# Optimization experiments

Measured on AMD Instinct MI355X. Metric: run time of the kernel, lower is better.

Reference implementation:

```python
import jax, jax.numpy as jnp
import numpy as np

B, H, D, V = 1024, 4, 128, 100000
EPS = 1e-7  # keras backend epsilon used by SparseCategoricalCrossentropy clipping


def setup_inputs() -> dict:
    key = jax.random.key(0)
    k0, k1, k2, k3, k4 = jax.random.split(key, 5)
    inputs = jax.random.normal(k0, (B, D), dtype=jnp.float32)
    label = jax.random.randint(k1, (B,), 0, V)
    embeddings = jax.random.normal(k2, (V, D), dtype=jnp.float32) * 0.05
    proj_mat = jax.random.normal(k3, (H * D, D), dtype=jnp.float32) * 0.05
    mix_mat = jax.random.normal(k4, (H, D), dtype=jnp.float32) * 0.05
    return {"inputs": inputs, "label": label, "embeddings": embeddings,
            "proj_mat": proj_mat, "mix_mat": mix_mat}


def reference(inputs, label, embeddings, proj_mat, mix_mat):
    # proj: [B, H*D] -> [B, H, D] with tanh nonlinearity
    proj = jnp.tanh(inputs @ proj_mat.T).reshape(-1, H, D)
    # mixture weights pi: [B, H]
    pi = jax.nn.softmax(inputs @ mix_mat.T, axis=-1)
    # per-head full-vocab logits/probs: [B, H, V]
    head_logits = jnp.einsum('bhd,vd->bhv', proj, embeddings)
    head_probs = jax.nn.softmax(head_logits, axis=-1)
    # mixture of softmaxes: [B, V]
    probs = jnp.einsum('bh,bhv->bv', pi, head_probs)
    # sparse categorical cross-entropy on probabilities (not logits)
    p_label = jnp.take_along_axis(probs, label[:, None], axis=1)[:, 0]
    loss = -jnp.mean(jnp.log(jnp.clip(p_label, EPS, 1.0)))
    return probs, loss
```

## Files before the change

kernel.cpp:

```cpp
#include <hip/hip_runtime.h>
#include <hip/hip_bf16.h>
#include <math.h>

#define B_ 1024
#define H_ 4
#define D_ 128
#define V_ 100000
#define M_ (B_*H_)
#define EPS_ 1e-7f

typedef unsigned short ushort_t;
typedef __attribute__((ext_vector_type(4))) float f32x4;
typedef __attribute__((ext_vector_type(8))) short bf16x8;

__device__ __forceinline__ ushort_t f2bf(float f) {
    unsigned u = __float_as_uint(f);
    unsigned r = u + 0x7fffu + ((u >> 16) & 1u);
    return (ushort_t)(r >> 16);
}

__device__ __forceinline__ void gload_lds16(const void* g, void* l) {
    __builtin_amdgcn_global_load_lds(
        (const __attribute__((address_space(1))) unsigned int*)g,
        (__attribute__((address_space(3))) unsigned int*)l,
        16, 0, 0);
}

__global__ __launch_bounds__(512)
void proj_pi_kernel(const float* __restrict__ inputs, const float* __restrict__ proj_mat,
                    const float* __restrict__ mix_mat, ushort_t* __restrict__ Abf,
                    float* __restrict__ pi)
{
    __shared__ float xin[128];
    __shared__ float mixv[4];
    const int b = blockIdx.x, tid = threadIdx.x;
    if (tid < 128) xin[tid] = inputs[b * 128 + tid];
    __syncthreads();

    const float4* row = (const float4*)(proj_mat + tid * 128);
    float acc = 0.f;
#pragma unroll 8
    for (int k = 0; k < 32; ++k) {
        float4 m4 = row[k];
        acc += m4.x * xin[k*4+0] + m4.y * xin[k*4+1] + m4.z * xin[k*4+2] + m4.w * xin[k*4+3];
    }
    Abf[b * 512 + tid] = f2bf(tanhf(acc));

    if (tid < 4) {
        const float4* mrow = (const float4*)(mix_mat + tid * 128);
        float a2 = 0.f;
#pragma unroll 8
        for (int k = 0; k < 32; ++k) {
            float4 m4 = mrow[k];
            a2 += m4.x * xin[k*4+0] + m4.y * xin[k*4+1] + m4.z * xin[k*4+2] + m4.w * xin[k*4+3];
        }
        mixv[tid] = a2;
    }
    __syncthreads();
    if (tid < 4) {
        float m = fmaxf(fmaxf(mixv[0], mixv[1]), fmaxf(mixv[2], mixv[3]));
        float e0 = __expf(mixv[0]-m), e1 = __expf(mixv[1]-m), e2 = __expf(mixv[2]-m), e3 = __expf(mixv[3]-m);
        float s = e0 + e1 + e2 + e3;
        float mye = __expf(mixv[tid]-m);
        pi[b * 4 + tid] = mye / s;
    }
}

__global__ __launch_bounds__(256)
void conv_kernel(const float* __restrict__ e, ushort_t* __restrict__ o, int n4)
{
    int i = blockIdx.x * 256 + threadIdx.x;
    if (i < n4) {
        float4 f = ((const float4*)e)[i];
        ushort4 u;
        u.x = f2bf(f.x); u.y = f2bf(f.y); u.z = f2bf(f.z); u.w = f2bf(f.w);
        ((ushort4*)o)[i] = u;
    }
}

template <int PASS>
__global__ __launch_bounds__(256, 2)
void gemm_kernel(const ushort_t* __restrict__ Abf, const ushort_t* __restrict__ Ebf,
                 const float* __restrict__ pi, float* __restrict__ Z,
                 float* __restrict__ probs)
{
    __shared__ ushort_t lds_a[128 * 128];
    __shared__ ushort_t lds_b[128 * 128];
    __shared__ float w_lds[128];

    const int tid  = threadIdx.x;
    const int wave = tid >> 6;
    const int lane = tid & 63;
    const int q    = lane >> 4;
    const int r16  = lane & 15;
    const int m0   = blockIdx.x * 128;
    const int v0   = blockIdx.y * 128;

    if (PASS == 2) {
        if (tid < 128) {
            int gi = m0 + tid;
            w_lds[tid] = pi[gi] / Z[gi];
        }
    }

#pragma unroll
    for (int t = 0; t < 8; ++t) {
        int r  = t * 16 + (tid >> 4);
        int c  = tid & 15;
        int cs = c ^ (r & 7);
        unsigned loff = (unsigned)__builtin_amdgcn_readfirstlane(t * 4096 + (tid >> 6) * 1024);
        gload_lds16(Abf + (size_t)(m0 + r) * 128 + cs * 8, (char*)lds_a + loff);
        int vrow = v0 + r; if (vrow >= V_) vrow = V_ - 1;
        gload_lds16(Ebf + (size_t)vrow * 128 + cs * 8, (char*)lds_b + loff);
    }
    __syncthreads();

    const int wm = (wave >> 1) * 64;
    const int wn = (wave & 1) * 64;

    f32x4 acc[4][4];
#pragma unroll
    for (int mi = 0; mi < 4; ++mi)
#pragma unroll
        for (int ni = 0; ni < 4; ++ni)
            acc[mi][ni] = (f32x4)(0.f);

#pragma unroll
    for (int kk = 0; kk < 4; ++kk) {
        bf16x8 fa[4], fb[4];
        int chunk = kk * 4 + q;
#pragma unroll
        for (int mi = 0; mi < 4; ++mi) {
            int row = wm + mi * 16 + r16;
            int sc = chunk ^ (row & 7);
            fa[mi] = *(const bf16x8*)&lds_a[row * 128 + sc * 8];
        }
#pragma unroll
        for (int ni = 0; ni < 4; ++ni) {
            int row = wn + ni * 16 + r16;
            int sc = chunk ^ (row & 7);
            fb[ni] = *(const bf16x8*)&lds_b[row * 128 + sc * 8];
        }
#pragma unroll
        for (int mi = 0; mi < 4; ++mi)
#pragma unroll
            for (int ni = 0; ni < 4; ++ni)
                acc[mi][ni] = __builtin_amdgcn_mfma_f32_16x16x32_bf16(fa[mi], fb[ni], acc[mi][ni], 0, 0, 0);
    }

    if (PASS == 1) {
        float zs[4][4];
#pragma unroll
        for (int mi = 0; mi < 4; ++mi)
#pragma unroll
            for (int h = 0; h < 4; ++h) zs[mi][h] = 0.f;

#pragma unroll
        for (int mi = 0; mi < 4; ++mi) {
#pragma unroll
            for (int ni = 0; ni < 4; ++ni) {
                int v = v0 + wn + ni * 16 + r16;
                bool ok = (v < V_);
#pragma unroll
                for (int h = 0; h < 4; ++h) {
                    float e = ok ? __expf(acc[mi][ni][h]) : 0.f;
                    zs[mi][h] += e;
                }
            }
        }
#pragma unroll
        for (int msk = 1; msk < 16; msk <<= 1) {
#pragma unroll
            for (int mi = 0; mi < 4; ++mi)
#pragma unroll
                for (int h = 0; h < 4; ++h)
                    zs[mi][h] += __shfl_xor(zs[mi][h], msk, 64);
        }
        int mi = r16 >> 2, h = r16 & 3;
        int midx = m0 + wm + mi * 16 + q * 4 + h;
        atomicAdd(&Z[midx], zs[mi][h]);
    } else {
#pragma unroll
        for (int mi = 0; mi < 4; ++mi) {
            int mloc = wm + mi * 16 + q * 4;
            float w0 = w_lds[mloc + 0], w1 = w_lds[mloc + 1];
            float w2 = w_lds[mloc + 2], w3 = w_lds[mloc + 3];
            size_t rowoff = (size_t)((m0 + mloc) >> 2) * V_;
#pragma unroll
            for (int ni = 0; ni < 4; ++ni) {
                int v = v0 + wn + ni * 16 + r16;
                if (v < V_) {
                    f32x4 a = acc[mi][ni];
                    float p = w0 * __expf(a[0]) + w1 * __expf(a[1])
                            + w2 * __expf(a[2]) + w3 * __expf(a[3]);
                    probs[rowoff + v] = p;
                }
            }
        }
    }
}

__global__ __launch_bounds__(256)
void loss_kernel(const float* __restrict__ probs, const int* __restrict__ label,
                 float* __restrict__ out)
{
    __shared__ float red[256];
    int tid = threadIdx.x;
    float s = 0.f;
    for (int b = tid; b < B_; b += 256) {
        float p = probs[(size_t)b * V_ + label[b]];
        p = fminf(fmaxf(p, EPS_), 1.0f);
        s -= logf(p);
    }
    red[tid] = s;
    __syncthreads();
    for (int st = 128; st > 0; st >>= 1) {
        if (tid < st) red[tid] += red[tid + st];
        __syncthreads();
    }
    if (tid == 0) out[0] = red[0] / (float)B_;
}

extern "C" void kernel_launch(void* const* d_in, const int* in_sizes, int n_in,
                              void* d_out, int out_size, void* d_ws, size_t ws_size,
                              hipStream_t stream)
{
    const float* inputs   = (const float*)d_in[0];
    const int*   label    = (const int*)d_in[1];
    const float* emb      = (const float*)d_in[2];
    const float* proj_mat = (const float*)d_in[3];
    const float* mix_mat  = (const float*)d_in[4];
    float* out = (float*)d_out;

    char* ws = (char*)d_ws;
    ushort_t* emb_bf = (ushort_t*)ws;
    ushort_t* A_bf   = (ushort_t*)(ws + 25600000);
    float*    pi     = (float*)(ws + 26648576);
    float*    Z      = (float*)(ws + 26664960);

    conv_kernel<<<12500, 256, 0, stream>>>(emb, emb_bf, 3200000);
    proj_pi_kernel<<<1024, 512, 0, stream>>>(inputs, proj_mat, mix_mat, A_bf, pi);
    hipMemsetAsync(Z, 0, 4096 * sizeof(float), stream);

    dim3 g(32, 782);
    gemm_kernel<1><<<g, 256, 0, stream>>>(A_bf, emb_bf, nullptr, Z, nullptr);
    gemm_kernel<2><<<g, 256, 0, stream>>>(A_bf, emb_bf, pi, Z, out);

    loss_kernel<<<1, 256, 0, stream>>>(out, label, out + (size_t)B_ * V_);
}
```

Measured before the change: 829.5 us.

## Replace two-pass GEMM with single pass storing bf16 exp scores plus combine kernel

The logits GEMM now runs once, writing per-head exp scores as bf16 to a padded workspace buffer while accumulating the softmax normalisers. A separate combine kernel then applies pi/Z weights to produce probs. This removes the second GEMM and exp pass. In exchange it adds a large intermediate buffer that must be written and read back, and it rounds the exp values to bf16. log2e is folded into the bf16 embeddings so exp2 can be used.

Measured after the change: 1.036 ms. 24.9% more time.

```diff
diff --git a/kernel.cpp b/kernel.cpp
--- a/kernel.cpp
+++ b/kernel.cpp
@@ -6,8 +6,10 @@
 #define H_ 4
 #define D_ 128
 #define V_ 100000
+#define VP_ 100096
 #define M_ (B_*H_)
 #define EPS_ 1e-7f
+#define LOG2E_ 1.4426950408889634f
 
 typedef unsigned short ushort_t;
 typedef __attribute__((ext_vector_type(4))) float f32x4;
@@ -18,6 +20,8 @@
     unsigned r = u + 0x7fffu + ((u >> 16) & 1u);
     return (ushort_t)(r >> 16);
 }
+__device__ __forceinline__ float bf_lo(unsigned x) { return __uint_as_float(x << 16); }
+__device__ __forceinline__ float bf_hi(unsigned x) { return __uint_as_float(x & 0xffff0000u); }
 
 __device__ __forceinline__ void gload_lds16(const void* g, void* l) {
     __builtin_amdgcn_global_load_lds(
@@ -61,8 +65,7 @@
         float m = fmaxf(fmaxf(mixv[0], mixv[1]), fmaxf(mixv[2], mixv[3]));
         float e0 = __expf(mixv[0]-m), e1 = __expf(mixv[1]-m), e2 = __expf(mixv[2]-m), e3 = __expf(mixv[3]-m);
         float s = e0 + e1 + e2 + e3;
-        float mye = __expf(mixv[tid]-m);
-        pi[b * 4 + tid] = mye / s;
+        pi[b * 4 + tid] = __expf(mixv[tid]-m) / s;
     }
 }
 
@@ -73,20 +76,18 @@
     if (i < n4) {
         float4 f = ((const float4*)e)[i];
         ushort4 u;
-        u.x = f2bf(f.x); u.y = f2bf(f.y); u.z = f2bf(f.z); u.w = f2bf(f.w);
+        u.x = f2bf(f.x * LOG2E_); u.y = f2bf(f.y * LOG2E_);
+        u.z = f2bf(f.z * LOG2E_); u.w = f2bf(f.w * LOG2E_);
         ((ushort4*)o)[i] = u;
     }
 }
 
-template <int PASS>
 __global__ __launch_bounds__(256, 2)
-void gemm_kernel(const ushort_t* __restrict__ Abf, const ushort_t* __restrict__ Ebf,
-                 const float* __restrict__ pi, float* __restrict__ Z,
-                 float* __restrict__ probs)
+void gemm_s_kernel(const ushort_t* __restrict__ Abf, const ushort_t* __restrict__ Ebf,
+                   ushort_t* __restrict__ S, float* __restrict__ Z)
 {
     __shared__ ushort_t lds_a[128 * 128];
     __shared__ ushort_t lds_b[128 * 128];
-    __shared__ float w_lds[128];
 
     const int tid  = threadIdx.x;
     const int wave = tid >> 6;
@@ -95,13 +96,6 @@
     const int r16  = lane & 15;
     const int m0   = blockIdx.x * 128;
     const int v0   = blockIdx.y * 128;
-
-    if (PASS == 2) {
-        if (tid < 128) {
-            int gi = m0 + tid;
-            w_lds[tid] = pi[gi] / Z[gi];
-        }
-    }
 
 #pragma unroll
     for (int t = 0; t < 8; ++t) {
@@ -148,56 +142,60 @@
                 acc[mi][ni] = __builtin_amdgcn_mfma_f32_16x16x32_bf16(fa[mi], fb[ni], acc[mi][ni], 0, 0, 0);
     }
 
-    if (PASS == 1) {
-        float zs[4][4];
+    float zs[4][4];
+#pragma unroll
+    for (int mi = 0; mi < 4; ++mi)
+#pragma unroll
+        for (int h = 0; h < 4; ++h) zs[mi][h] = 0.f;
+
+#pragma unroll
+    for (int mi = 0; mi < 4; ++mi) {
+        int bidx = (m0 + wm + mi * 16) / 4 + q;
+#pragma unroll
+        for (int ni = 0; ni < 4; ++ni) {
+            int v = v0 + wn + ni * 16 + r16;
+            f32x4 a = acc[mi][ni];
+            float e0 = exp2f(a[0]), e1 = exp2f(a[1]), e2 = exp2f(a[2]), e3 = exp2f(a[3]);
+            ushort4 s4;
+            s4.x = f2bf(e0); s4.y = f2bf(e1); s4.z = f2bf(e2); s4.w = f2bf(e3);
+            *(ushort4*)(S + ((size_t)bidx * VP_ + v) * 4) = s4;
+            if (v < V_) {
+                zs[mi][0] += e0; zs[mi][1] += e1; zs[mi][2] += e2; zs[mi][3] += e3;
+            }
+        }
+    }
+#pragma unroll
+    for (int msk = 1; msk < 16; msk <<= 1) {
 #pragma unroll
         for (int mi = 0; mi < 4; ++mi)
 #pragma unroll
-            for (int h = 0; h < 4; ++h) zs[mi][h] = 0.f;
-
-#pragma unroll
-        for (int mi = 0; mi < 4; ++mi) {
-#pragma unroll
-            for (int ni = 0; ni < 4; ++ni) {
-                int v = v0 + wn + ni * 16 + r16;
-                bool ok = (v < V_);
-#pragma unroll
-                for (int h = 0; h < 4; ++h) {
-                    float e = ok ? __expf(acc[mi][ni][h]) : 0.f;
-                    zs[mi][h] += e;
-                }
-            }
-        }
-#pragma unroll
-        for (int msk = 1; msk < 16; msk <<= 1) {
-#pragma unroll
-            for (int mi = 0; mi < 4; ++mi)
-#pragma unroll
-                for (int h = 0; h < 4; ++h)
-                    zs[mi][h] += __shfl_xor(zs[mi][h], msk, 64);
-        }
-        int mi = r16 >> 2, h = r16 & 3;
-        int midx = m0 + wm + mi * 16 + q * 4 + h;
-        atomicAdd(&Z[midx], zs[mi][h]);
-    } else {
-#pragma unroll
-        for (int mi = 0; mi < 4; ++mi) {
-            int mloc = wm + mi * 16 + q * 4;
-            float w0 = w_lds[mloc + 0], w1 = w_lds[mloc + 1];
-            float w2 = w_lds[mloc + 2], w3 = w_lds[mloc + 3];
-            size_t rowoff = (size_t)((m0 + mloc) >> 2) * V_;
-#pragma unroll
-            for (int ni = 0; ni < 4; ++ni) {
-                int v = v0 + wn + ni * 16 + r16;
-                if (v < V_) {
-                    f32x4 a = acc[mi][ni];
-                    float p = w0 * __expf(a[0]) + w1 * __expf(a[1])
-                            + w2 * __expf(a[2]) + w3 * __expf(a[3]);
-                    probs[rowoff + v] = p;
-                }
-            }
-        }
-    }
+            for (int h = 0; h < 4; ++h)
+                zs[mi][h] += __shfl_xor(zs[mi][h], msk, 64);
+    }
+    int mi = r16 >> 2, h = r16 & 3;
+    int midx = m0 + wm + mi * 16 + q * 4 + h;
+    atomicAdd(&Z[midx], zs[mi][h]);
+}
+
+__global__ __launch_bounds__(256)
+void combine_kernel(const ushort_t* __restrict__ S, const float* __restrict__ pi,
+                    const float* __restrict__ Z, float* __restrict__ probs)
+{
+    __shared__ float w[4];
+    const int b = blockIdx.y;
+    if (threadIdx.x < 4) w[threadIdx.x] = pi[b * 4 + threadIdx.x] / Z[b * 4 + threadIdx.x];
+    __syncthreads();
+    int v = (blockIdx.x * 256 + threadIdx.x) * 4;
+    if (v >= V_) return;
+    const uint4* sp = (const uint4*)(S + ((size_t)b * VP_ + v) * 4);
+    uint4 sa = sp[0], sb = sp[1];
+    float w0 = w[0], w1 = w[1], w2 = w[2], w3 = w[3];
+    float4 r;
+    r.x = w0 * bf_lo(sa.x) + w1 * bf_hi(sa.x) + w2 * bf_lo(sa.y) + w3 * bf_hi(sa.y);
+    r.y = w0 * bf_lo(sa.z) + w1 * bf_hi(sa.z) + w2 * bf_lo(sa.w) + w3 * bf_hi(sa.w);
+    r.z = w0 * bf_lo(sb.x) + w1 * bf_hi(sb.x) + w2 * bf_lo(sb.y) + w3 * bf_hi(sb.y);
+    r.w = w0 * bf_lo(sb.z) + w1 * bf_hi(sb.z) + w2 * bf_lo(sb.w) + w3 * bf_hi(sb.w);
+    *(float4*)(probs + (size_t)b * V_ + v) = r;
 }
 
 __global__ __launch_bounds__(256)
@@ -237,14 +235,17 @@
     ushort_t* A_bf   = (ushort_t*)(ws + 25600000);
     float*    pi     = (float*)(ws + 26648576);
     float*    Z      = (float*)(ws + 26664960);
+    ushort_t* S      = (ushort_t*)(ws + 33554432);
 
     conv_kernel<<<12500, 256, 0, stream>>>(emb, emb_bf, 3200000);
     proj_pi_kernel<<<1024, 512, 0, stream>>>(inputs, proj_mat, mix_mat, A_bf, pi);
     hipMemsetAsync(Z, 0, 4096 * sizeof(float), stream);
 
     dim3 g(32, 782);
-    gemm_kernel<1><<<g, 256, 0, stream>>>(A_bf, emb_bf, nullptr, Z, nullptr);
-    gemm_kernel<2><<<g, 256, 0, stream>>>(A_bf, emb_bf, pi, Z, out);
+    gemm_s_kernel<<<g, 256, 0, stream>>>(A_bf, emb_bf, S, Z);
+
+    dim3 gc(98, 1024);
+    combine_kernel<<<gc, 256, 0, stream>>>(S, pi, Z, out);
 
     loss_kernel<<<1, 256, 0, stream>>>(out, label, out + (size_t)B_ * V_);
 }
```
